# Performance work log

Hardware: AMD Instinct MI355X
Metric: run time of the kernel (lower is better)

Reference implementation:

```python
import jax, jax.numpy as jnp
import numpy as np

N_PER_GRAPH = 32
DEGREE = 8
N_GRAPHS = 2048
IN_CH = 64
HID = 64
OUT = 4
EPS = 1e-5


def setup_inputs() -> dict:
    key = jax.random.key(0)
    ks = jax.random.split(key, 12)
    N = N_GRAPHS * N_PER_GRAPH
    # ring connectivity: node i -> (i+d) mod 32 within each graph, d=1..DEGREE
    i = np.arange(N_PER_GRAPH)
    offs = np.arange(1, DEGREE + 1)
    s = np.repeat(i, DEGREE)
    d = (s + np.tile(offs, N_PER_GRAPH)) % N_PER_GRAPH
    base = (np.arange(N_GRAPHS) * N_PER_GRAPH)[:, None]
    src = (base + s[None, :]).reshape(-1)
    dst = (base + d[None, :]).reshape(-1)
    edge_index = jnp.asarray(np.stack([src, dst]).astype(np.int32))
    batch = jnp.asarray((np.arange(N) // N_PER_GRAPH).astype(np.int32))

    def w(k, shape, fan_in):
        return jax.random.normal(k, shape, jnp.float32) / np.float32(np.sqrt(fan_in))

    return dict(
        x=jax.random.normal(ks[0], (N, IN_CH), jnp.float32),
        edge_weight=jax.random.uniform(ks[1], (edge_index.shape[1],), jnp.float32),
        W1a=w(ks[2], (IN_CH, HID), IN_CH), W1b=w(ks[3], (IN_CH, HID), IN_CH),
        b1=jnp.zeros((HID,), jnp.float32), g1=jnp.ones((HID,), jnp.float32), be1=jnp.zeros((HID,), jnp.float32),
        W2a=w(ks[4], (HID, 2 * HID), HID), W2b=w(ks[5], (HID, 2 * HID), HID),
        b2=jnp.zeros((2 * HID,), jnp.float32), g2=jnp.ones((2 * HID,), jnp.float32), be2=jnp.zeros((2 * HID,), jnp.float32),
        W3a=w(ks[6], (2 * HID, 2 * HID), 2 * HID), W3b=w(ks[7], (2 * HID, 2 * HID), 2 * HID),
        b3=jnp.zeros((2 * HID,), jnp.float32), g3=jnp.ones((2 * HID,), jnp.float32), be3=jnp.zeros((2 * HID,), jnp.float32),
        fcW=w(ks[8], (2 * HID, OUT), 2 * HID), fcb=jnp.zeros((OUT,), jnp.float32),
        edge_index=edge_index, batch=batch,
    )


def cheb_conv(x, src, dst, ew, W0, W1, b):
    # PyG ChebConv, K=2, sym normalization, lambda_max=2:
    # scaled Laplacian L_hat = L - I = -D^{-1/2} A D^{-1/2} (diag exactly 0)
    n = x.shape[0]
    deg = jnp.zeros((n,), x.dtype).at[src].add(ew)
    dinv = jnp.where(deg > 0, jax.lax.rsqrt(deg), 0.0)
    norm = -dinv[src] * ew * dinv[dst]
    tx1 = jnp.zeros_like(x).at[dst].add(norm[:, None] * x[src])  # [n, C] gather-scatter
    return x @ W0 + tx1 @ W1 + b


def batch_norm(x, g, b):
    # training-mode BatchNorm over the node dimension (biased variance, as torch)
    m = x.mean(0)
    v = x.var(0)
    return (x - m) * jax.lax.rsqrt(v + EPS) * g + b


def pool_half(x, src, dst, ew):
    # deterministic stand-in for graclus: pair consecutive nodes (pairs stay
    # within a graph since each graph has an even node count).
    n = x.shape[0]
    cluster = jnp.arange(n) // 2
    x2 = jax.ops.segment_max(x, cluster, num_segments=n // 2)
    s2, d2 = src // 2, dst // 2
    # zero-weight self loops == removing them (contribute 0 to degree & messages);
    # keeping duplicate edges == coalescing with sum under segment_sum ops.
    ew2 = jnp.where(s2 == d2, jnp.zeros_like(ew), ew)
    return x2, s2, d2, ew2


def forward(x, edge_weight, W1a, W1b, b1, g1, be1, W2a, W2b, b2, g2, be2,
            W3a, W3b, b3, g3, be3, fcW, fcb, edge_index, batch):
    src, dst = edge_index[0], edge_index[1]
    ew = edge_weight
    h = jax.nn.softplus(batch_norm(cheb_conv(x, src, dst, ew, W1a, W1b, b1), g1, be1))
    h, src, dst, ew = pool_half(h, src, dst, ew)
    h = jax.nn.softplus(batch_norm(cheb_conv(h, src, dst, ew, W2a, W2b, b2), g2, be2))
    h, src, dst, ew = pool_half(h, src, dst, ew)
    h = jax.nn.softplus(batch_norm(cheb_conv(h, src, dst, ew, W3a, W3b, b3), g3, be3))
    batch3 = batch[::4]  # batch vector after two halvings of consecutive pairs
    sums = jax.ops.segment_sum(h, batch3, num_segments=N_GRAPHS)
    cnt = jax.ops.segment_sum(jnp.ones((h.shape[0],), h.dtype), batch3, num_segments=N_GRAPHS)
    hg = sums / jnp.maximum(cnt, 1.0)[:, None]
    return jax.nn.log_softmax(hg @ fcW + fcb, axis=1)


def reference(x, edge_weight, W1a, W1b, b1, g1, be1, W2a, W2b, b2, g2, be2,
              W3a, W3b, b3, g3, be3, fcW, fcb, edge_index, batch):
    return forward(x, edge_weight, W1a, W1b, b1, g1, be1, W2a, W2b, b2, g2, be2,
                   W3a, W3b, b3, g3, be3, fcW, fcb, edge_index, batch)
```

## Files before the change

kernel.cpp:

```cpp
#include <hip/hip_runtime.h>

#define EPSV 1e-5f

typedef __attribute__((ext_vector_type(8))) short short8;
typedef __attribute__((ext_vector_type(4))) float f32x4;

__device__ __forceinline__ float softplus_f(float x){
    return fmaxf(x, 0.f) + log1pf(expf(-fabsf(x)));
}
__device__ __forceinline__ float bf2f(short u){
    union{unsigned int i; float f;} x; x.i = ((unsigned int)(unsigned short)u) << 16; return x.f;
}
__device__ __forceinline__ short f2bf(float f){
    union{float f; unsigned int i;} x; x.f = f;
    unsigned int r = x.i + 0x7fffu + ((x.i >> 16) & 1u);
    return (short)(r >> 16);
}

#define W1TA_OFF 0
#define W1TB_OFF 4608
#define W2TA_OFF 9216
#define W2TB_OFF 18432
#define W3TA_OFF 27648
#define W3TB_OFF 45056
#define WT_TOTAL 62464

__global__ void k_prep(const float* __restrict__ W1a, const float* __restrict__ W1b,
                       const float* __restrict__ W2a, const float* __restrict__ W2b,
                       const float* __restrict__ W3a, const float* __restrict__ W3b,
                       short* __restrict__ wt){
    int blk = blockIdx.x, tid = threadIdx.x;
    const float* src; short* dst; int N, SP, base;
    if      (blk < 16){  src = W1a; dst = wt + W1TA_OFF; N = 64;  SP = 72;  base = blk; }
    else if (blk < 32){  src = W1b; dst = wt + W1TB_OFF; N = 64;  SP = 72;  base = blk - 16; }
    else if (blk < 64){  src = W2a; dst = wt + W2TA_OFF; N = 128; SP = 72;  base = blk - 32; }
    else if (blk < 96){  src = W2b; dst = wt + W2TB_OFF; N = 128; SP = 72;  base = blk - 64; }
    else if (blk < 160){ src = W3a; dst = wt + W3TA_OFF; N = 128; SP = 136; base = blk - 96; }
    else              {  src = W3b; dst = wt + W3TB_OFF; N = 128; SP = 136; base = blk - 160; }
    int e = base * 256 + tid;
    int k = e / N, c = e % N;
    dst[c * SP + k] = f2bf(src[e]);
}

__global__ __launch_bounds__(256) void k_conv1(const float* __restrict__ x, const float* __restrict__ ew,
        const short* __restrict__ w1ta, const short* __restrict__ w1tb,
        const float* __restrict__ b1, short* __restrict__ h1){
    __shared__ float ews[256], nrm[256], dinv[32];
    __shared__ __align__(16) short xsb[32][72];
    __shared__ __align__(16) short tsb[32][72];
    __shared__ __align__(16) short wla[64][72];
    __shared__ __align__(16) short wlb[64][72];
    int g = blockIdx.x, tid = threadIdx.x;
    ews[tid] = ew[(size_t)g*256 + tid];
    {
        const float4* xg = (const float4*)(x + (size_t)g*32*64);
        #pragma unroll
        for (int p = 0; p < 2; ++p){
            int i4 = tid + p*256;
            int r = i4 >> 4, cc = (i4 & 15)*4;
            float4 v = xg[i4];
            xsb[r][cc+0] = f2bf(v.x); xsb[r][cc+1] = f2bf(v.y);
            xsb[r][cc+2] = f2bf(v.z); xsb[r][cc+3] = f2bf(v.w);
        }
    }
    {
        int c = tid >> 2, k0 = (tid & 3)*16;
        *(short8*)&wla[c][k0]   = *(const short8*)&w1ta[c*72 + k0];
        *(short8*)&wla[c][k0+8] = *(const short8*)&w1ta[c*72 + k0 + 8];
        *(short8*)&wlb[c][k0]   = *(const short8*)&w1tb[c*72 + k0];
        *(short8*)&wlb[c][k0+8] = *(const short8*)&w1tb[c*72 + k0 + 8];
    }
    __syncthreads();
    if (tid < 32){
        float d = 0.f;
        #pragma unroll
        for (int k = 0; k < 8; ++k) d += ews[tid*8 + k];
        dinv[tid] = d > 0.f ? rsqrtf(d) : 0.f;
    }
    __syncthreads();
    {   int se = tid >> 3, de = (se + (tid & 7) + 1) & 31;
        nrm[tid] = -dinv[se] * ews[tid] * dinv[de]; }
    __syncthreads();
    {
        int v = tid >> 3, ch = (tid & 7)*8;
        float acc[8];
        #pragma unroll
        for (int j = 0; j < 8; ++j) acc[j] = 0.f;
        #pragma unroll
        for (int k = 0; k < 8; ++k){
            int sl = (v - k - 1) & 31;
            float nw = nrm[sl*8 + k];
            short8 xv = *(const short8*)&xsb[sl][ch];
            #pragma unroll
            for (int j = 0; j < 8; ++j) acc[j] = fmaf(nw, bf2f(xv[j]), acc[j]);
        }
        short8 o;
        #pragma unroll
        for (int j = 0; j < 8; ++j) o[j] = f2bf(acc[j]);
        *(short8*)&tsb[v][ch] = o;
    }
    __syncthreads();
    int lane = tid & 63, w = tid >> 6;
    int lrow = lane & 15, lk8 = lane >> 4;
    int rt = w & 1, cp = w >> 1;
    f32x4 acc0 = {0,0,0,0}, acc1 = {0,0,0,0};
    #pragma unroll
    for (int ks = 0; ks < 2; ++ks){
        int kb = ks*32 + lk8*8;
        short8 ax  = *(const short8*)&xsb[rt*16 + lrow][kb];
        short8 at  = *(const short8*)&tsb[rt*16 + lrow][kb];
        short8 b0a = *(const short8*)&wla[cp*32 + lrow][kb];
        short8 b0b = *(const short8*)&wlb[cp*32 + lrow][kb];
        short8 b1a = *(const short8*)&wla[cp*32 + 16 + lrow][kb];
        short8 b1b = *(const short8*)&wlb[cp*32 + 16 + lrow][kb];
        acc0 = __builtin_amdgcn_mfma_f32_16x16x32_bf16(ax, b0a, acc0, 0, 0, 0);
        acc0 = __builtin_amdgcn_mfma_f32_16x16x32_bf16(at, b0b, acc0, 0, 0, 0);
        acc1 = __builtin_amdgcn_mfma_f32_16x16x32_bf16(ax, b1a, acc1, 0, 0, 0);
        acc1 = __builtin_amdgcn_mfma_f32_16x16x32_bf16(at, b1b, acc1, 0, 0, 0);
    }
    {   int c0 = cp*32 + lrow, c1 = c0 + 16;
        float bb0 = b1[c0], bb1 = b1[c1];
        size_t rowbase = (size_t)g*32 + rt*16 + lk8*4;
        #pragma unroll
        for (int e2 = 0; e2 < 4; ++e2){
            h1[(rowbase + e2)*64 + c0] = f2bf(acc0[e2] + bb0);
            h1[(rowbase + e2)*64 + c1] = f2bf(acc1[e2] + bb1);
        }
    }
}

__global__ __launch_bounds__(256) void k_conv2(const short* __restrict__ h1, const float* __restrict__ ew,
        const float* __restrict__ sum1, const float* __restrict__ sq1,
        const float* __restrict__ g1, const float* __restrict__ be1,
        const short* __restrict__ w2ta, const short* __restrict__ w2tb,
        const float* __restrict__ b2, short* __restrict__ h2){
    __shared__ float ews[256], nrm[256], dinv[16];
    __shared__ float scl[64], sft[64];
    __shared__ __align__(16) short xpb[16][72];
    __shared__ __align__(16) short tsb[16][72];
    __shared__ __align__(16) short wla[128][72];
    __shared__ __align__(16) short wlb[128][72];
    int g = blockIdx.x, tid = threadIdx.x;
    ews[tid] = ew[(size_t)g*256 + tid];
    if (tid < 64){
        float m = sum1[tid] * (1.f/65536.f);
        float v = sq1[tid] * (1.f/65536.f) - m*m;
        float rs = rsqrtf(v + EPSV) * g1[tid];
        scl[tid] = rs; sft[tid] = be1[tid] - m*rs;
    }
    {   int c = tid >> 1, k0 = (tid & 1)*32;
        #pragma unroll
        for (int p = 0; p < 4; ++p){
            *(short8*)&wla[c][k0 + p*8] = *(const short8*)&w2ta[c*72 + k0 + p*8];
            *(short8*)&wlb[c][k0 + p*8] = *(const short8*)&w2tb[c*72 + k0 + p*8];
        }
    }
    __syncthreads();
    if (tid < 128){
        int vo = tid >> 3, ch = (tid & 7)*8;
        short8 a = *(const short8*)&h1[((size_t)g*32 + 2*vo)*64 + ch];
        short8 b = *(const short8*)&h1[((size_t)g*32 + 2*vo + 1)*64 + ch];
        short8 o;
        #pragma unroll
        for (int j = 0; j < 8; ++j){
            float s = scl[ch+j], t = sft[ch+j];
            float va = softplus_f(bf2f(a[j])*s + t);
            float vb = softplus_f(bf2f(b[j])*s + t);
            o[j] = f2bf(fmaxf(va, vb));
        }
        *(short8*)&xpb[vo][ch] = o;
    }
    if (tid < 16){
        float d = 0.f;
        for (int t = tid*16; t < tid*16 + 16; ++t){
            int se = t >> 3, de = (se + (t & 7) + 1) & 31;
            float wv = ((se >> 1) == (de >> 1)) ? 0.f : ews[t];
            d += wv;
        }
        dinv[tid] = d > 0.f ? rsqrtf(d) : 0.f;
    }
    __syncthreads();
    {   int se = tid >> 3, de = (se + (tid & 7) + 1) & 31;
        float wv = ((se >> 1) == (de >> 1)) ? 0.f : ews[tid];
        nrm[tid] = -dinv[se >> 1] * wv * dinv[de >> 1]; }
    __syncthreads();
    if (tid < 128){
        int v = tid >> 3, ch = (tid & 7)*8;
        float acc[8];
        #pragma unroll
        for (int j = 0; j < 8; ++j) acc[j] = 0.f;
        #pragma unroll
        for (int dd = 0; dd < 2; ++dd){
            int d = v*2 + dd;
            #pragma unroll
            for (int k = 0; k < 8; ++k){
                int sl = (d - k - 1) & 31;
                float nw = nrm[sl*8 + k];
                short8 xv = *(const short8*)&xpb[sl >> 1][ch];
                #pragma unroll
                for (int j = 0; j < 8; ++j) acc[j] = fmaf(nw, bf2f(xv[j]), acc[j]);
            }
        }
        short8 o;
        #pragma unroll
        for (int j = 0; j < 8; ++j) o[j] = f2bf(acc[j]);
        *(short8*)&tsb[v][ch] = o;
    }
    __syncthreads();
    int lane = tid & 63, w = tid >> 6, lrow = lane & 15, lk8 = lane >> 4;
    f32x4 acc0 = {0,0,0,0}, acc1 = {0,0,0,0};
    #pragma unroll
    for (int ks = 0; ks < 2; ++ks){
        int kb = ks*32 + lk8*8;
        short8 ax  = *(const short8*)&xpb[lrow][kb];
        short8 at  = *(const short8*)&tsb[lrow][kb];
        short8 b0a = *(const short8*)&wla[w*32 + lrow][kb];
        short8 b0b = *(const short8*)&wlb[w*32 + lrow][kb];
        short8 b1a = *(const short8*)&wla[w*32 + 16 + lrow][kb];
        short8 b1b = *(const short8*)&wlb[w*32 + 16 + lrow][kb];
        acc0 = __builtin_amdgcn_mfma_f32_16x16x32_bf16(ax, b0a, acc0, 0, 0, 0);
        acc0 = __builtin_amdgcn_mfma_f32_16x16x32_bf16(at, b0b, acc0, 0, 0, 0);
        acc1 = __builtin_amdgcn_mfma_f32_16x16x32_bf16(ax, b1a, acc1, 0, 0, 0);
        acc1 = __builtin_amdgcn_mfma_f32_16x16x32_bf16(at, b1b, acc1, 0, 0, 0);
    }
    {   int c0 = w*32 + lrow, c1 = c0 + 16;
        float bb0 = b2[c0], bb1 = b2[c1];
        size_t rowbase = (size_t)g*16 + lk8*4;
        #pragma unroll
        for (int e2 = 0; e2 < 4; ++e2){
            h2[(rowbase + e2)*128 + c0] = f2bf(acc0[e2] + bb0);
            h2[(rowbase + e2)*128 + c1] = f2bf(acc1[e2] + bb1);
        }
    }
}

__global__ __launch_bounds__(256) void k_conv3(const short* __restrict__ h2, const float* __restrict__ ew,
        const float* __restrict__ sum2, const float* __restrict__ sq2,
        const float* __restrict__ g2, const float* __restrict__ be2,
        const short* __restrict__ w3ta, const short* __restrict__ w3tb,
        const float* __restrict__ b3, short* __restrict__ h3){
    __shared__ float ews[256], nrm[256], dinv[8];
    __shared__ float scl[128], sft[128];
    __shared__ __align__(16) short xpb[16][136];
    __shared__ __align__(16) short tsb[16][136];
    __shared__ __align__(16) short wca[64][136];
    __shared__ __align__(16) short wcb[64][136];
    int g = blockIdx.x, tid = threadIdx.x;
    ews[tid] = ew[(size_t)g*256 + tid];
    if (tid < 128){
        float m = sum2[tid] * (1.f/32768.f);
        float v = sq2[tid] * (1.f/32768.f) - m*m;
        float rs = rsqrtf(v + EPSV) * g2[tid];
        scl[tid] = rs; sft[tid] = be2[tid] - m*rs;
    }
    for (int idx = tid; idx < 8*136; idx += 256){
        int r = 8 + idx/136, c = idx % 136;
        xpb[r][c] = 0; tsb[r][c] = 0;
    }
    __syncthreads();
    if (tid < 128){
        int vo = tid >> 4, ch = (tid & 15)*8;
        short8 a = *(const short8*)&h2[((size_t)g*16 + 2*vo)*128 + ch];
        short8 b = *(const short8*)&h2[((size_t)g*16 + 2*vo + 1)*128 + ch];
        short8 o;
        #pragma unroll
        for (int j = 0; j < 8; ++j){
            float s = scl[ch+j], t = sft[ch+j];
            float va = softplus_f(bf2f(a[j])*s + t);
            float vb = softplus_f(bf2f(b[j])*s + t);
            o[j] = f2bf(fmaxf(va, vb));
        }
        *(short8*)&xpb[vo][ch] = o;
    }
    if (tid < 8){
        float d = 0.f;
        for (int t = tid*32; t < tid*32 + 32; ++t){
            int se = t >> 3, de = (se + (t & 7) + 1) & 31;
            float wv = ((se >> 2) == (de >> 2)) ? 0.f : ews[t];
            d += wv;
        }
        dinv[tid] = d > 0.f ? rsqrtf(d) : 0.f;
    }
    __syncthreads();
    {   int se = tid >> 3, de = (se + (tid & 7) + 1) & 31;
        float wv = ((se >> 2) == (de >> 2)) ? 0.f : ews[tid];
        nrm[tid] = -dinv[se >> 2] * wv * dinv[de >> 2]; }
    __syncthreads();
    if (tid < 128){
        int v = tid >> 4, ch = (tid & 15)*8;
        float acc[8];
        #pragma unroll
        for (int j = 0; j < 8; ++j) acc[j] = 0.f;
        #pragma unroll
        for (int dd = 0; dd < 4; ++dd){
            int d = v*4 + dd;
            #pragma unroll
            for (int k = 0; k < 8; ++k){
                int sl = (d - k - 1) & 31;
                float nw = nrm[sl*8 + k];
                short8 xv = *(const short8*)&xpb[sl >> 2][ch];
                #pragma unroll
                for (int j = 0; j < 8; ++j) acc[j] = fmaf(nw, bf2f(xv[j]), acc[j]);
            }
        }
        short8 o;
        #pragma unroll
        for (int j = 0; j < 8; ++j) o[j] = f2bf(acc[j]);
        *(short8*)&tsb[v][ch] = o;
    }
    __syncthreads();
    int lane = tid & 63, w = tid >> 6, lrow = lane & 15, lk8 = lane >> 4;
    short8 ax[4], at[4];
    #pragma unroll
    for (int ks = 0; ks < 4; ++ks){
        int kb = ks*32 + lk8*8;
        ax[ks] = *(const short8*)&xpb[lrow][kb];
        at[ks] = *(const short8*)&tsb[lrow][kb];
    }
    #pragma unroll
    for (int cc = 0; cc < 2; ++cc){
        {   int c = tid >> 2, k0 = (tid & 3)*32;
            const short* pa = w3ta + ((size_t)(cc*64 + c))*136 + k0;
            const short* pb = w3tb + ((size_t)(cc*64 + c))*136 + k0;
            #pragma unroll
            for (int p = 0; p < 4; ++p){
                *(short8*)&wca[c][k0 + p*8] = *(const short8*)(pa + p*8);
                *(short8*)&wcb[c][k0 + p*8] = *(const short8*)(pb + p*8);
            }
        }
        __syncthreads();
        f32x4 acc = {0,0,0,0};
        #pragma unroll
        for (int ks = 0; ks < 4; ++ks){
            int kb = ks*32 + lk8*8;
            short8 ba = *(const short8*)&wca[w*16 + lrow][kb];
            short8 bb = *(const short8*)&wcb[w*16 + lrow][kb];
            acc = __builtin_amdgcn_mfma_f32_16x16x32_bf16(ax[ks], ba, acc, 0, 0, 0);
            acc = __builtin_amdgcn_mfma_f32_16x16x32_bf16(at[ks], bb, acc, 0, 0, 0);
        }
        if (lk8 < 2){
            int col = cc*64 + w*16 + lrow;
            float bb0 = b3[col];
            #pragma unroll
            for (int e2 = 0; e2 < 4; ++e2){
                int row = lk8*4 + e2;
                h3[((size_t)g*8 + row)*128 + col] = f2bf(acc[e2] + bb0);
            }
        }
        __syncthreads();
    }
}

template<int C>
__global__ void k_stats_bf(const short* __restrict__ h, float* __restrict__ sums,
                           float* __restrict__ sumsq, int total8){
    __shared__ float ls[C], lq[C];
    int tid = threadIdx.x;
    for (int i = tid; i < C; i += 256){ ls[i] = 0.f; lq[i] = 0.f; }
    __syncthreads();
    int T = gridDim.x * 256;
    float s[8], q[8];
    #pragma unroll
    for (int j = 0; j < 8; ++j){ s[j] = 0.f; q[j] = 0.f; }
    int i0 = blockIdx.x*256 + tid;
    for (int i = i0; i < total8; i += T){
        short8 v = *(const short8*)&h[(size_t)i*8];
        #pragma unroll
        for (int j = 0; j < 8; ++j){ float f = bf2f(v[j]); s[j] += f; q[j] += f*f; }
    }
    int cb = (i0*8) % C;
    #pragma unroll
    for (int j = 0; j < 8; ++j){ atomicAdd(&ls[cb+j], s[j]); atomicAdd(&lq[cb+j], q[j]); }
    __syncthreads();
    for (int i = tid; i < C; i += 256){
        atomicAdd(&sums[i],  ls[i]);
        atomicAdd(&sumsq[i], lq[i]);
    }
}

__global__ void k_head_bf(const short* __restrict__ h3, const float* __restrict__ sums,
        const float* __restrict__ sumsq, const float* __restrict__ gamma,
        const float* __restrict__ beta, const float* __restrict__ fcW,
        const float* __restrict__ fcb, float* __restrict__ out){
    __shared__ float4 part[128];
    int g = blockIdx.x, c = threadIdx.x;
    const float nl_inv = 1.f/16384.f;
    float m = sums[c] * nl_inv;
    float var = sumsq[c] * nl_inv - m*m;
    float rstd = rsqrtf(var + EPSV);
    float ga = gamma[c], be = beta[c];
    float acc = 0.f;
    #pragma unroll
    for (int nn = 0; nn < 8; ++nn){
        float z = bf2f(h3[((size_t)g*8 + nn)*128 + c]);
        acc += softplus_f((z - m)*rstd*ga + be);
    }
    float hg = acc * 0.125f;
    float4 w = *(reinterpret_cast<const float4*>(fcW) + c);
    part[c] = make_float4(hg*w.x, hg*w.y, hg*w.z, hg*w.w);
    __syncthreads();
    for (int s = 64; s > 0; s >>= 1){
        if (c < s){
            float4 o = part[c + s];
            part[c].x += o.x; part[c].y += o.y; part[c].z += o.z; part[c].w += o.w;
        }
        __syncthreads();
    }
    if (c == 0){
        float z0 = part[0].x + fcb[0], z1 = part[0].y + fcb[1];
        float z2 = part[0].z + fcb[2], z3 = part[0].w + fcb[3];
        float mx = fmaxf(fmaxf(z0, z1), fmaxf(z2, z3));
        float lse = mx + logf(expf(z0-mx) + expf(z1-mx) + expf(z2-mx) + expf(z3-mx));
        float* o = out + (size_t)g*4;
        o[0] = z0 - lse; o[1] = z1 - lse; o[2] = z2 - lse; o[3] = z3 - lse;
    }
}

extern "C" void kernel_launch(void* const* d_in, const int* in_sizes, int n_in,
                              void* d_out, int out_size, void* d_ws, size_t ws_size,
                              hipStream_t stream){
    const float* x   = (const float*)d_in[0];
    const float* ew  = (const float*)d_in[1];
    const float* W1a = (const float*)d_in[2];
    const float* W1b = (const float*)d_in[3];
    const float* b1  = (const float*)d_in[4];
    const float* g1  = (const float*)d_in[5];
    const float* be1 = (const float*)d_in[6];
    const float* W2a = (const float*)d_in[7];
    const float* W2b = (const float*)d_in[8];
    const float* b2  = (const float*)d_in[9];
    const float* g2  = (const float*)d_in[10];
    const float* be2 = (const float*)d_in[11];
    const float* W3a = (const float*)d_in[12];
    const float* W3b = (const float*)d_in[13];
    const float* b3  = (const float*)d_in[14];
    const float* g3  = (const float*)d_in[15];
    const float* be3 = (const float*)d_in[16];
    const float* fcW = (const float*)d_in[17];
    const float* fcb = (const float*)d_in[18];
    float* out = (float*)d_out;
    (void)in_sizes; (void)n_in; (void)out_size; (void)ws_size;

    short* h1 = (short*)d_ws;
    short* h2 = h1 + (size_t)4194304;
    short* h3 = h2 + (size_t)4194304;
    short* wT = h3 + (size_t)2097152;
    float* st = (float*)(((uintptr_t)(wT + WT_TOTAL) + 255) & ~(uintptr_t)255);
    float* sum1 = st,        *sq1 = st + 64;
    float* sum2 = st + 128,  *sq2 = st + 256;
    float* sum3 = st + 384,  *sq3 = st + 512;

    hipMemsetAsync(st, 0, 640*sizeof(float), stream);
    k_prep<<<224, 256, 0, stream>>>(W1a, W1b, W2a, W2b, W3a, W3b, wT);

    k_conv1<<<2048, 256, 0, stream>>>(x, ew, wT + W1TA_OFF, wT + W1TB_OFF, b1, h1);
    k_stats_bf<64><<<256, 256, 0, stream>>>(h1, sum1, sq1, 524288);

    k_conv2<<<2048, 256, 0, stream>>>(h1, ew, sum1, sq1, g1, be1,
                                      wT + W2TA_OFF, wT + W2TB_OFF, b2, h2);
    k_stats_bf<128><<<256, 256, 0, stream>>>(h2, sum2, sq2, 524288);

    k_conv3<<<2048, 256, 0, stream>>>(h2, ew, sum2, sq2, g2, be2,
                                      wT + W3TA_OFF, wT + W3TB_OFF, b3, h3);
    k_stats_bf<128><<<256, 256, 0, stream>>>(h3, sum3, sq3, 262144);

    k_head_bf<<<2048, 128, 0, stream>>>(h3, sum3, sq3, g3, be3, fcW, fcb, out);
}
```

Before: 223.5 us.

## Split gather and GEMM stages, fuse BN statistics into tiled MFMA GEMM

Each per-graph conv kernel is split into a gather kernel, which writes the bf16 node features and the Chebyshev term to global memory, and a separate tiled GEMM kernel. The GEMM handles 64-128 rows per block, so each block loads the weights once for many graphs, and it emits per-block BatchNorm partial sums; a small reduce kernel then turns these into scale and shift, replacing the atomic stats passes and the memset. The head kernel now handles one graph per wavefront and reduces with shuffles. The trade-off is extra global round-trips for the intermediate xb/tx buffers and more kernel launches.

```diff
diff --git a/kernel.cpp b/kernel.cpp
--- a/kernel.cpp
+++ b/kernel.cpp
@@ -42,18 +42,13 @@
     dst[c * SP + k] = f2bf(src[e]);
 }
 
-__global__ __launch_bounds__(256) void k_conv1(const float* __restrict__ x, const float* __restrict__ ew,
-        const short* __restrict__ w1ta, const short* __restrict__ w1tb,
-        const float* __restrict__ b1, short* __restrict__ h1){
+__global__ __launch_bounds__(256) void k_gat1(const float* __restrict__ x, const float* __restrict__ ew,
+        short* __restrict__ xb1, short* __restrict__ tx1){
     __shared__ float ews[256], nrm[256], dinv[32];
     __shared__ __align__(16) short xsb[32][72];
-    __shared__ __align__(16) short tsb[32][72];
-    __shared__ __align__(16) short wla[64][72];
-    __shared__ __align__(16) short wlb[64][72];
     int g = blockIdx.x, tid = threadIdx.x;
     ews[tid] = ew[(size_t)g*256 + tid];
-    {
-        const float4* xg = (const float4*)(x + (size_t)g*32*64);
+    {   const float4* xg = (const float4*)(x + (size_t)g*32*64);
         #pragma unroll
         for (int p = 0; p < 2; ++p){
             int i4 = tid + p*256;
@@ -63,13 +58,6 @@
             xsb[r][cc+2] = f2bf(v.z); xsb[r][cc+3] = f2bf(v.w);
         }
     }
-    {
-        int c = tid >> 2, k0 = (tid & 3)*16;
-        *(short8*)&wla[c][k0]   = *(const short8*)&w1ta[c*72 + k0];
-        *(short8*)&wla[c][k0+8] = *(const short8*)&w1ta[c*72 + k0 + 8];
-        *(short8*)&wlb[c][k0]   = *(const short8*)&w1tb[c*72 + k0];
-        *(short8*)&wlb[c][k0+8] = *(const short8*)&w1tb[c*72 + k0 + 8];
-    }
     __syncthreads();
     if (tid < 32){
         float d = 0.f;
@@ -81,80 +69,34 @@
     {   int se = tid >> 3, de = (se + (tid & 7) + 1) & 31;
         nrm[tid] = -dinv[se] * ews[tid] * dinv[de]; }
     __syncthreads();
-    {
-        int v = tid >> 3, ch = (tid & 7)*8;
-        float acc[8];
-        #pragma unroll
-        for (int j = 0; j < 8; ++j) acc[j] = 0.f;
-        #pragma unroll
-        for (int k = 0; k < 8; ++k){
-            int sl = (v - k - 1) & 31;
-            float nw = nrm[sl*8 + k];
-            short8 xv = *(const short8*)&xsb[sl][ch];
-            #pragma unroll
-            for (int j = 0; j < 8; ++j) acc[j] = fmaf(nw, bf2f(xv[j]), acc[j]);
-        }
-        short8 o;
-        #pragma unroll
-        for (int j = 0; j < 8; ++j) o[j] = f2bf(acc[j]);
-        *(short8*)&tsb[v][ch] = o;
-    }
-    __syncthreads();
-    int lane = tid & 63, w = tid >> 6;
-    int lrow = lane & 15, lk8 = lane >> 4;
-    int rt = w & 1, cp = w >> 1;
-    f32x4 acc0 = {0,0,0,0}, acc1 = {0,0,0,0};
-    #pragma unroll
-    for (int ks = 0; ks < 2; ++ks){
-        int kb = ks*32 + lk8*8;
-        short8 ax  = *(const short8*)&xsb[rt*16 + lrow][kb];
-        short8 at  = *(const short8*)&tsb[rt*16 + lrow][kb];
-        short8 b0a = *(const short8*)&wla[cp*32 + lrow][kb];
-        short8 b0b = *(const short8*)&wlb[cp*32 + lrow][kb];
-        short8 b1a = *(const short8*)&wla[cp*32 + 16 + lrow][kb];
-        short8 b1b = *(const short8*)&wlb[cp*32 + 16 + lrow][kb];
-        acc0 = __builtin_amdgcn_mfma_f32_16x16x32_bf16(ax, b0a, acc0, 0, 0, 0);
-        acc0 = __builtin_amdgcn_mfma_f32_16x16x32_bf16(at, b0b, acc0, 0, 0, 0);
-        acc1 = __builtin_amdgcn_mfma_f32_16x16x32_bf16(ax, b1a, acc1, 0, 0, 0);
-        acc1 = __builtin_amdgcn_mfma_f32_16x16x32_bf16(at, b1b, acc1, 0, 0, 0);
-    }
-    {   int c0 = cp*32 + lrow, c1 = c0 + 16;
-        float bb0 = b1[c0], bb1 = b1[c1];
-        size_t rowbase = (size_t)g*32 + rt*16 + lk8*4;
-        #pragma unroll
-        for (int e2 = 0; e2 < 4; ++e2){
-            h1[(rowbase + e2)*64 + c0] = f2bf(acc0[e2] + bb0);
-            h1[(rowbase + e2)*64 + c1] = f2bf(acc1[e2] + bb1);
-        }
-    }
-}
-
-__global__ __launch_bounds__(256) void k_conv2(const short* __restrict__ h1, const float* __restrict__ ew,
-        const float* __restrict__ sum1, const float* __restrict__ sq1,
-        const float* __restrict__ g1, const float* __restrict__ be1,
-        const short* __restrict__ w2ta, const short* __restrict__ w2tb,
-        const float* __restrict__ b2, short* __restrict__ h2){
+    int v = tid >> 3, ch = (tid & 7)*8;
+    *(short8*)&xb1[((size_t)g*32 + v)*64 + ch] = *(const short8*)&xsb[v][ch];
+    float acc[8];
+    #pragma unroll
+    for (int j = 0; j < 8; ++j) acc[j] = 0.f;
+    #pragma unroll
+    for (int k = 0; k < 8; ++k){
+        int sl = (v - k - 1) & 31;
+        float nw = nrm[sl*8 + k];
+        short8 xv = *(const short8*)&xsb[sl][ch];
+        #pragma unroll
+        for (int j = 0; j < 8; ++j) acc[j] = fmaf(nw, bf2f(xv[j]), acc[j]);
+    }
+    short8 o;
+    #pragma unroll
+    for (int j = 0; j < 8; ++j) o[j] = f2bf(acc[j]);
+    *(short8*)&tx1[((size_t)g*32 + v)*64 + ch] = o;
+}
+
+__global__ __launch_bounds__(256) void k_gat2(const short* __restrict__ h1, const float* __restrict__ ew,
+        const float* __restrict__ scl1, const float* __restrict__ sft1,
+        short* __restrict__ xb2, short* __restrict__ tx2){
     __shared__ float ews[256], nrm[256], dinv[16];
     __shared__ float scl[64], sft[64];
     __shared__ __align__(16) short xpb[16][72];
-    __shared__ __align__(16) short tsb[16][72];
-    __shared__ __align__(16) short wla[128][72];
-    __shared__ __align__(16) short wlb[128][72];
     int g = blockIdx.x, tid = threadIdx.x;
     ews[tid] = ew[(size_t)g*256 + tid];
-    if (tid < 64){
-        float m = sum1[tid] * (1.f/65536.f);
-        float v = sq1[tid] * (1.f/65536.f) - m*m;
-        float rs = rsqrtf(v + EPSV) * g1[tid];
-        scl[tid] = rs; sft[tid] = be1[tid] - m*rs;
-    }
-    {   int c = tid >> 1, k0 = (tid & 1)*32;
-        #pragma unroll
-        for (int p = 0; p < 4; ++p){
-            *(short8*)&wla[c][k0 + p*8] = *(const short8*)&w2ta[c*72 + k0 + p*8];
-            *(short8*)&wlb[c][k0 + p*8] = *(const short8*)&w2tb[c*72 + k0 + p*8];
-        }
-    }
+    if (tid < 64){ scl[tid] = scl1[tid]; sft[tid] = sft1[tid]; }
     __syncthreads();
     if (tid < 128){
         int vo = tid >> 3, ch = (tid & 7)*8;
@@ -169,6 +111,7 @@
             o[j] = f2bf(fmaxf(va, vb));
         }
         *(short8*)&xpb[vo][ch] = o;
+        *(short8*)&xb2[((size_t)g*16 + vo)*64 + ch] = o;
     }
     if (tid < 16){
         float d = 0.f;
@@ -204,59 +147,19 @@
         short8 o;
         #pragma unroll
         for (int j = 0; j < 8; ++j) o[j] = f2bf(acc[j]);
-        *(short8*)&tsb[v][ch] = o;
-    }
-    __syncthreads();
-    int lane = tid & 63, w = tid >> 6, lrow = lane & 15, lk8 = lane >> 4;
-    f32x4 acc0 = {0,0,0,0}, acc1 = {0,0,0,0};
-    #pragma unroll
-    for (int ks = 0; ks < 2; ++ks){
-        int kb = ks*32 + lk8*8;
-        short8 ax  = *(const short8*)&xpb[lrow][kb];
-        short8 at  = *(const short8*)&tsb[lrow][kb];
-        short8 b0a = *(const short8*)&wla[w*32 + lrow][kb];
-        short8 b0b = *(const short8*)&wlb[w*32 + lrow][kb];
-        short8 b1a = *(const short8*)&wla[w*32 + 16 + lrow][kb];
-        short8 b1b = *(const short8*)&wlb[w*32 + 16 + lrow][kb];
-        acc0 = __builtin_amdgcn_mfma_f32_16x16x32_bf16(ax, b0a, acc0, 0, 0, 0);
-        acc0 = __builtin_amdgcn_mfma_f32_16x16x32_bf16(at, b0b, acc0, 0, 0, 0);
-        acc1 = __builtin_amdgcn_mfma_f32_16x16x32_bf16(ax, b1a, acc1, 0, 0, 0);
-        acc1 = __builtin_amdgcn_mfma_f32_16x16x32_bf16(at, b1b, acc1, 0, 0, 0);
-    }
-    {   int c0 = w*32 + lrow, c1 = c0 + 16;
-        float bb0 = b2[c0], bb1 = b2[c1];
-        size_t rowbase = (size_t)g*16 + lk8*4;
-        #pragma unroll
-        for (int e2 = 0; e2 < 4; ++e2){
-            h2[(rowbase + e2)*128 + c0] = f2bf(acc0[e2] + bb0);
-            h2[(rowbase + e2)*128 + c1] = f2bf(acc1[e2] + bb1);
-        }
-    }
-}
-
-__global__ __launch_bounds__(256) void k_conv3(const short* __restrict__ h2, const float* __restrict__ ew,
-        const float* __restrict__ sum2, const float* __restrict__ sq2,
-        const float* __restrict__ g2, const float* __restrict__ be2,
-        const short* __restrict__ w3ta, const short* __restrict__ w3tb,
-        const float* __restrict__ b3, short* __restrict__ h3){
+        *(short8*)&tx2[((size_t)g*16 + v)*64 + ch] = o;
+    }
+}
+
+__global__ __launch_bounds__(256) void k_gat3(const short* __restrict__ h2, const float* __restrict__ ew,
+        const float* __restrict__ scl2, const float* __restrict__ sft2,
+        short* __restrict__ xb3, short* __restrict__ tx3){
     __shared__ float ews[256], nrm[256], dinv[8];
     __shared__ float scl[128], sft[128];
-    __shared__ __align__(16) short xpb[16][136];
-    __shared__ __align__(16) short tsb[16][136];
-    __shared__ __align__(16) short wca[64][136];
-    __shared__ __align__(16) short wcb[64][136];
+    __shared__ __align__(16) short xpb[8][136];
     int g = blockIdx.x, tid = threadIdx.x;
     ews[tid] = ew[(size_t)g*256 + tid];
-    if (tid < 128){
-        float m = sum2[tid] * (1.f/32768.f);
-        float v = sq2[tid] * (1.f/32768.f) - m*m;
-        float rs = rsqrtf(v + EPSV) * g2[tid];
-        scl[tid] = rs; sft[tid] = be2[tid] - m*rs;
-    }
-    for (int idx = tid; idx < 8*136; idx += 256){
-        int r = 8 + idx/136, c = idx % 136;
-        xpb[r][c] = 0; tsb[r][c] = 0;
-    }
+    if (tid < 128){ scl[tid] = scl2[tid]; sft[tid] = sft2[tid]; }
     __syncthreads();
     if (tid < 128){
         int vo = tid >> 4, ch = (tid & 15)*8;
@@ -271,6 +174,7 @@
             o[j] = f2bf(fmaxf(va, vb));
         }
         *(short8*)&xpb[vo][ch] = o;
+        *(short8*)&xb3[((size_t)g*8 + vo)*128 + ch] = o;
     }
     if (tid < 8){
         float d = 0.f;
@@ -306,113 +210,152 @@
         short8 o;
         #pragma unroll
         for (int j = 0; j < 8; ++j) o[j] = f2bf(acc[j]);
-        *(short8*)&tsb[v][ch] = o;
-    }
-    __syncthreads();
+        *(short8*)&tx3[((size_t)g*8 + v)*128 + ch] = o;
+    }
+}
+
+template<int BM, int CIN, int COUT, int NB>
+__global__ __launch_bounds__(256) void k_gemm(const short* __restrict__ xb, const short* __restrict__ tx,
+        const short* __restrict__ Wa, const short* __restrict__ Wb, int WSP,
+        const float* __restrict__ bias, short* __restrict__ h, float* __restrict__ P){
+    constexpr int RPW = BM/4, RT = RPW/16, CT = COUT/16, KC = CIN/64;
+    __shared__ __align__(16) short As[BM][72];
+    __shared__ __align__(16) short Bs[COUT][72];
+    __shared__ float ssum[COUT], ssq[COUT];
+    int blk = blockIdx.x, tid = threadIdx.x;
     int lane = tid & 63, w = tid >> 6, lrow = lane & 15, lk8 = lane >> 4;
-    short8 ax[4], at[4];
-    #pragma unroll
-    for (int ks = 0; ks < 4; ++ks){
-        int kb = ks*32 + lk8*8;
-        ax[ks] = *(const short8*)&xpb[lrow][kb];
-        at[ks] = *(const short8*)&tsb[lrow][kb];
-    }
-    #pragma unroll
-    for (int cc = 0; cc < 2; ++cc){
-        {   int c = tid >> 2, k0 = (tid & 3)*32;
-            const short* pa = w3ta + ((size_t)(cc*64 + c))*136 + k0;
-            const short* pb = w3tb + ((size_t)(cc*64 + c))*136 + k0;
+    if (tid < COUT){ ssum[tid] = 0.f; ssq[tid] = 0.f; }
+    f32x4 acc[RT][CT];
+    #pragma unroll
+    for (int rt = 0; rt < RT; ++rt)
+        #pragma unroll
+        for (int ct = 0; ct < CT; ++ct) acc[rt][ct] = (f32x4){0,0,0,0};
+
+    #pragma unroll
+    for (int seg = 0; seg < 2; ++seg){
+        const short* Ag = seg ? tx : xb;
+        const short* Wg = seg ? Wb : Wa;
+        #pragma unroll
+        for (int kc = 0; kc < KC; ++kc){
+            __syncthreads();
+            for (int idx = tid; idx < BM*8; idx += 256){
+                int r = idx >> 3, ko = (idx & 7)*8;
+                *(short8*)&As[r][ko] =
+                    *(const short8*)&Ag[((size_t)(blk*BM + r))*CIN + kc*64 + ko];
+            }
+            for (int idx = tid; idx < COUT*8; idx += 256){
+                int c = idx >> 3, ko = (idx & 7)*8;
+                *(short8*)&Bs[c][ko] =
+                    *(const short8*)&Wg[(size_t)c*WSP + kc*64 + ko];
+            }
+            __syncthreads();
             #pragma unroll
-            for (int p = 0; p < 4; ++p){
-                *(short8*)&wca[c][k0 + p*8] = *(const short8*)(pa + p*8);
-                *(short8*)&wcb[c][k0 + p*8] = *(const short8*)(pb + p*8);
-            }
-        }
+            for (int ks = 0; ks < 2; ++ks){
+                short8 af[RT];
+                #pragma unroll
+                for (int rt = 0; rt < RT; ++rt)
+                    af[rt] = *(const short8*)&As[w*RPW + rt*16 + lrow][ks*32 + lk8*8];
+                #pragma unroll
+                for (int ct = 0; ct < CT; ++ct){
+                    short8 bf = *(const short8*)&Bs[ct*16 + lrow][ks*32 + lk8*8];
+                    #pragma unroll
+                    for (int rt = 0; rt < RT; ++rt)
+                        acc[rt][ct] = __builtin_amdgcn_mfma_f32_16x16x32_bf16(af[rt], bf, acc[rt][ct], 0, 0, 0);
+                }
+            }
+        }
+    }
+    #pragma unroll
+    for (int ct = 0; ct < CT; ++ct){
+        int col = ct*16 + lrow;
+        float bb = bias[col];
+        float s = 0.f, q = 0.f;
+        #pragma unroll
+        for (int rt = 0; rt < RT; ++rt){
+            #pragma unroll
+            for (int e = 0; e < 4; ++e){
+                float v = acc[rt][ct][e] + bb;
+                int row = blk*BM + w*RPW + rt*16 + lk8*4 + e;
+                h[(size_t)row*COUT + col] = f2bf(v);
+                s += v; q += v*v;
+            }
+        }
+        s += __shfl_xor(s, 16); s += __shfl_xor(s, 32);
+        q += __shfl_xor(q, 16); q += __shfl_xor(q, 32);
+        if (lane < 16){ atomicAdd(&ssum[col], s); atomicAdd(&ssq[col], q); }
+    }
+    __syncthreads();
+    if (tid < COUT){
+        P[(size_t)tid*NB + blk]          = ssum[tid];
+        P[(size_t)(COUT + tid)*NB + blk] = ssq[tid];
+    }
+}
+
+template<int C, int NB>
+__global__ void k_red(const float* __restrict__ P, const float* __restrict__ gamma,
+                      const float* __restrict__ beta, float nl_inv,
+                      float* __restrict__ scl, float* __restrict__ sft){
+    __shared__ float r1[128], r2[128];
+    int c = blockIdx.x, t = threadIdx.x;
+    if (t < 128){
+        float s = 0.f;
+        for (int i = t; i < NB; i += 128) s += P[(size_t)c*NB + i];
+        r1[t] = s;
+    } else {
+        float q = 0.f;
+        for (int i = t - 128; i < NB; i += 128) q += P[(size_t)(C + c)*NB + i];
+        r2[t - 128] = q;
+    }
+    __syncthreads();
+    for (int s = 64; s > 0; s >>= 1){
+        if (t < s) r1[t] += r1[t + s];
+        else if (t >= 128 && t - 128 < s) r2[t - 128] += r2[t - 128 + s];
         __syncthreads();
-        f32x4 acc = {0,0,0,0};
-        #pragma unroll
-        for (int ks = 0; ks < 4; ++ks){
-            int kb = ks*32 + lk8*8;
-            short8 ba = *(const short8*)&wca[w*16 + lrow][kb];
-            short8 bb = *(const short8*)&wcb[w*16 + lrow][kb];
-            acc = __builtin_amdgcn_mfma_f32_16x16x32_bf16(ax[ks], ba, acc, 0, 0, 0);
-            acc = __builtin_amdgcn_mfma_f32_16x16x32_bf16(at[ks], bb, acc, 0, 0, 0);
-        }
-        if (lk8 < 2){
-            int col = cc*64 + w*16 + lrow;
-            float bb0 = b3[col];
-            #pragma unroll
-            for (int e2 = 0; e2 < 4; ++e2){
-                int row = lk8*4 + e2;
-                h3[((size_t)g*8 + row)*128 + col] = f2bf(acc[e2] + bb0);
-            }
-        }
-        __syncthreads();
-    }
-}
-
-template<int C>
-__global__ void k_stats_bf(const short* __restrict__ h, float* __restrict__ sums,
-                           float* __restrict__ sumsq, int total8){
-    __shared__ float ls[C], lq[C];
-    int tid = threadIdx.x;
-    for (int i = tid; i < C; i += 256){ ls[i] = 0.f; lq[i] = 0.f; }
-    __syncthreads();
-    int T = gridDim.x * 256;
-    float s[8], q[8];
-    #pragma unroll
-    for (int j = 0; j < 8; ++j){ s[j] = 0.f; q[j] = 0.f; }
-    int i0 = blockIdx.x*256 + tid;
-    for (int i = i0; i < total8; i += T){
-        short8 v = *(const short8*)&h[(size_t)i*8];
-        #pragma unroll
-        for (int j = 0; j < 8; ++j){ float f = bf2f(v[j]); s[j] += f; q[j] += f*f; }
-    }
-    int cb = (i0*8) % C;
-    #pragma unroll
-    for (int j = 0; j < 8; ++j){ atomicAdd(&ls[cb+j], s[j]); atomicAdd(&lq[cb+j], q[j]); }
-    __syncthreads();
-    for (int i = tid; i < C; i += 256){
-        atomicAdd(&sums[i],  ls[i]);
-        atomicAdd(&sumsq[i], lq[i]);
-    }
-}
-
-__global__ void k_head_bf(const short* __restrict__ h3, const float* __restrict__ sums,
-        const float* __restrict__ sumsq, const float* __restrict__ gamma,
-        const float* __restrict__ beta, const float* __restrict__ fcW,
-        const float* __restrict__ fcb, float* __restrict__ out){
-    __shared__ float4 part[128];
-    int g = blockIdx.x, c = threadIdx.x;
-    const float nl_inv = 1.f/16384.f;
-    float m = sums[c] * nl_inv;
-    float var = sumsq[c] * nl_inv - m*m;
-    float rstd = rsqrtf(var + EPSV);
-    float ga = gamma[c], be = beta[c];
-    float acc = 0.f;
-    #pragma unroll
-    for (int nn = 0; nn < 8; ++nn){
-        float z = bf2f(h3[((size_t)g*8 + nn)*128 + c]);
-        acc += softplus_f((z - m)*rstd*ga + be);
-    }
-    float hg = acc * 0.125f;
-    float4 w = *(reinterpret_cast<const float4*>(fcW) + c);
-    part[c] = make_float4(hg*w.x, hg*w.y, hg*w.z, hg*w.w);
-    __syncthreads();
-    for (int s = 64; s > 0; s >>= 1){
-        if (c < s){
-            float4 o = part[c + s];
-            part[c].x += o.x; part[c].y += o.y; part[c].z += o.z; part[c].w += o.w;
-        }
-        __syncthreads();
-    }
-    if (c == 0){
-        float z0 = part[0].x + fcb[0], z1 = part[0].y + fcb[1];
-        float z2 = part[0].z + fcb[2], z3 = part[0].w + fcb[3];
+    }
+    if (t == 0){
+        float m = r1[0] * nl_inv;
+        float var = r2[0] * nl_inv - m*m;
+        float rs = rsqrtf(var + EPSV) * gamma[c];
+        scl[c] = rs;
+        sft[c] = beta[c] - m*rs;
+    }
+}
+
+__global__ __launch_bounds__(256) void k_head(const short* __restrict__ h3,
+        const float* __restrict__ scl3, const float* __restrict__ sft3,
+        const float* __restrict__ fcW, const float* __restrict__ fcb,
+        float* __restrict__ out){
+    int tid = threadIdx.x, w = tid >> 6, lane = tid & 63;
+    int g = blockIdx.x*4 + w;
+    int c0 = lane*2;
+    float sc0 = scl3[c0], sh0 = sft3[c0];
+    float sc1 = scl3[c0+1], sh1 = sft3[c0+1];
+    float acc0 = 0.f, acc1 = 0.f;
+    #pragma unroll
+    for (int n = 0; n < 8; ++n){
+        unsigned int v = *(const unsigned int*)&h3[((size_t)g*8 + n)*128 + c0];
+        union{unsigned int i; float f;} lo, hi;
+        lo.i = v << 16; hi.i = v & 0xffff0000u;
+        acc0 += softplus_f(lo.f*sc0 + sh0);
+        acc1 += softplus_f(hi.f*sc1 + sh1);
+    }
+    float hg0 = acc0 * 0.125f, hg1 = acc1 * 0.125f;
+    float4 w0 = ((const float4*)fcW)[c0];
+    float4 w1 = ((const float4*)fcW)[c0+1];
+    float z0 = hg0*w0.x + hg1*w1.x;
+    float z1 = hg0*w0.y + hg1*w1.y;
+    float z2 = hg0*w0.z + hg1*w1.z;
+    float z3 = hg0*w0.w + hg1*w1.w;
+    #pragma unroll
+    for (int d = 1; d < 64; d <<= 1){
+        z0 += __shfl_xor(z0, d); z1 += __shfl_xor(z1, d);
+        z2 += __shfl_xor(z2, d); z3 += __shfl_xor(z3, d);
+    }
+    if (lane == 0){
+        z0 += fcb[0]; z1 += fcb[1]; z2 += fcb[2]; z3 += fcb[3];
         float mx = fmaxf(fmaxf(z0, z1), fmaxf(z2, z3));
         float lse = mx + logf(expf(z0-mx) + expf(z1-mx) + expf(z2-mx) + expf(z3-mx));
-        float* o = out + (size_t)g*4;
-        o[0] = z0 - lse; o[1] = z1 - lse; o[2] = z2 - lse; o[3] = z3 - lse;
+        *(float4*)(out + (size_t)g*4) = make_float4(z0-lse, z1-lse, z2-lse, z3-lse);
     }
 }
 
@@ -441,28 +384,37 @@
     float* out = (float*)d_out;
     (void)in_sizes; (void)n_in; (void)out_size; (void)ws_size;
 
-    short* h1 = (short*)d_ws;
-    short* h2 = h1 + (size_t)4194304;
-    short* h3 = h2 + (size_t)4194304;
-    short* wT = h3 + (size_t)2097152;
-    float* st = (float*)(((uintptr_t)(wT + WT_TOTAL) + 255) & ~(uintptr_t)255);
-    float* sum1 = st,        *sq1 = st + 64;
-    float* sum2 = st + 128,  *sq2 = st + 256;
-    float* sum3 = st + 384,  *sq3 = st + 512;
-
-    hipMemsetAsync(st, 0, 640*sizeof(float), stream);
+    short* xb1 = (short*)d_ws;
+    short* tx1 = xb1 + (size_t)4194304;
+    short* h1  = tx1 + (size_t)4194304;
+    short* xb2 = h1  + (size_t)4194304;
+    short* tx2 = xb2 + (size_t)2097152;
+    short* h2  = tx2 + (size_t)2097152;
+    short* xb3 = h2  + (size_t)4194304;
+    short* tx3 = xb3 + (size_t)2097152;
+    short* h3  = tx3 + (size_t)2097152;
+    short* wT  = h3  + (size_t)2097152;
+    float* fp  = (float*)(((uintptr_t)(wT + WT_TOTAL) + 255) & ~(uintptr_t)255);
+    float* P1  = fp;
+    float* P2  = P1 + 65536;
+    float* P3  = P2 + 65536;
+    float* scl1 = P3 + 65536;  float* sft1 = scl1 + 64;
+    float* scl2 = sft1 + 64;   float* sft2 = scl2 + 128;
+    float* scl3 = sft2 + 128;  float* sft3 = scl3 + 128;
+
     k_prep<<<224, 256, 0, stream>>>(W1a, W1b, W2a, W2b, W3a, W3b, wT);
 
-    k_conv1<<<2048, 256, 0, stream>>>(x, ew, wT + W1TA_OFF, wT + W1TB_OFF, b1, h1);
-    k_stats_bf<64><<<256, 256, 0, stream>>>(h1, sum1, sq1, 524288);
-
-    k_conv2<<<2048, 256, 0, stream>>>(h1, ew, sum1, sq1, g1, be1,
-                                      wT + W2TA_OFF, wT + W2TB_OFF, b2, h2);
-    k_stats_bf<128><<<256, 256, 0, stream>>>(h2, sum2, sq2, 524288);
-
-    k_conv3<<<2048, 256, 0, stream>>>(h2, ew, sum2, sq2, g2, be2,
-                                      wT + W3TA_OFF, wT + W3TB_OFF, b3, h3);
-    k_stats_bf<128><<<256, 256, 0, stream>>>(h3, sum3, sq3, 262144);
-
-    k_head_bf<<<2048, 128, 0, stream>>>(h3, sum3, sq3, g3, be3, fcW, fcb, out);
-}
+    k_gat1<<<2048, 256, 0, stream>>>(x, ew, xb1, tx1);
+    k_gemm<128,64,64,512><<<512, 256, 0, stream>>>(xb1, tx1, wT + W1TA_OFF, wT + W1TB_OFF, 72, b1, h1, P1);
+    k_red<64,512><<<64, 256, 0, stream>>>(P1, g1, be1, 1.f/65536.f, scl1, sft1);
+
+    k_gat2<<<2048, 256, 0, stream>>>(h1, ew, scl1, sft1, xb2, tx2);
+    k_gemm<128,64,128,256><<<256, 256, 0, stream>>>(xb2, tx2, wT + W2TA_OFF, wT + W2TB_OFF, 72, b2, h2, P2);
+    k_red<128,256><<<128, 256, 0, stream>>>(P2, g2, be2, 1.f/32768.f, scl2, sft2);
+
+    k_gat3<<<2048, 256, 0, stream>>>(h2, ew, scl2, sft2, xb3, tx3);
+    k_gemm<64,128,128,256><<<256, 256, 0, stream>>>(xb3, tx3, wT + W3TA_OFF, wT + W3TB_OFF, 136, b3, h3, P3);
+    k_red<128,256><<<128, 256, 0, stream>>>(P3, g3, be3, 1.f/16384.f, scl3, sft3);
+
+    k_head<<<512, 256, 0, stream>>>(h3, scl3, sft3, fcW, fcb, out);
+}
```

Result: faster. 214.7 us (-3.9%).
